# Kernel tuning notes

Hardware: AMD Instinct MI355X
Metric: run time of the kernel (lower is better)

Reference implementation:

```python
import jax, jax.numpy as jnp
import numpy as np
import math

NB = 3            # anchors per level
NC = 80           # classes
NET = 640.0       # net input size
STRIDES = (8.0, 16.0, 32.0)
ANCHORS = np.array([[12,16],[19,36],[40,28],[36,75],[76,55],[72,146],
                    [142,110],[192,243],[459,401]], dtype=np.float32)
MASKS = np.array([[0,1,2],[3,4,5],[6,7,8]], dtype=np.int32)
SCALE_XY = (2.0, 2.0, 2.0)
BALANCE = (4.0, 1.0, 0.4)
IOU_NORM = 0.05
OBJ_NORM = 0.7 * (NET / 640.0) ** 2
CLS_NORM = 0.3 * NC / 80.0
ANCHOR_T = 4.0
G = 0.5           # append_g offset threshold
EPS = 1e-7


def _bce(logits, t):
    # BCEWithLogits, elementwise: (1-t)*x + softplus(-x)
    return (1.0 - t) * logits + jax.nn.softplus(-logits)


def _ciou(box1, box2):
    # boxes are (cx, cy, w, h); returns CIoU, shape = broadcast of leading dims
    x1, y1, w1, h1 = box1[..., 0], box1[..., 1], box1[..., 2], box1[..., 3]
    x2, y2, w2, h2 = box2[..., 0], box2[..., 1], box2[..., 2], box2[..., 3]
    b1x1, b1x2 = x1 - w1 * 0.5, x1 + w1 * 0.5
    b1y1, b1y2 = y1 - h1 * 0.5, y1 + h1 * 0.5
    b2x1, b2x2 = x2 - w2 * 0.5, x2 + w2 * 0.5
    b2y1, b2y2 = y2 - h2 * 0.5, y2 + h2 * 0.5
    inter = (jnp.clip(jnp.minimum(b1x2, b2x2) - jnp.maximum(b1x1, b2x1), 0.0) *
             jnp.clip(jnp.minimum(b1y2, b2y2) - jnp.maximum(b1y1, b2y1), 0.0))
    union = w1 * h1 + w2 * h2 - inter + EPS
    iou = inter / union
    cw = jnp.maximum(b1x2, b2x2) - jnp.minimum(b1x1, b2x1)
    ch = jnp.maximum(b1y2, b2y2) - jnp.minimum(b1y1, b2y1)
    c2 = cw * cw + ch * ch + EPS
    rho2 = ((b2x1 + b2x2 - b1x1 - b1x2) ** 2 + (b2y1 + b2y2 - b1y1 - b1y2) ** 2) / 4.0
    v = (4.0 / math.pi ** 2) * (jnp.arctan(w2 / (h2 + EPS)) - jnp.arctan(w1 / (h1 + EPS))) ** 2
    alpha = jax.lax.stop_gradient(v / (v - iou + (1.0 + EPS)))
    return iou - (rho2 / c2 + v * alpha)


def _build_targets(targets, nb, S, idx):
    # vectorized version of the per-target python loop: for each target,
    # up to 5 grid cells (center + 4 offsets) x A anchor-ratio matches.
    b = targets[:, 0].astype(jnp.int32)          # [N]
    cls = targets[:, 1].astype(jnp.int32)        # [N]
    box = targets[:, 2:6]                        # [N,4] normalized xywh
    N = box.shape[0]
    A = NB
    anch = jnp.asarray(ANCHORS[MASKS[idx]] / STRIDES[idx])   # [A,2] grid units
    wh = box[:, 2:4] * S                                     # [N,2]
    r = wh[:, None, :] / anch[None, :, :]                    # [N,A,2]
    rmatch = jnp.max(jnp.maximum(r, 1.0 / r), axis=-1) < ANCHOR_T  # [N,A]
    gx, gy = box[:, 0] * S, box[:, 1] * S
    ib = jnp.floor(gx).astype(jnp.int32)
    jb = jnp.floor(gy).astype(jnp.int32)
    oi, oj = gx % 1.0, gy % 1.0
    pos = jnp.stack([
        jnp.ones_like(gx, dtype=bool),
        (oi < G) & (gx > 1.0),
        (oj < G) & (gy > 1.0),
        (oi > G) & (S - gx > 1.0),
        (oj > G) & (S - gy > 1.0)], axis=1)                  # [N,5]
    di = jnp.array([0, -1, 0, 1, 0], dtype=jnp.int32)
    dj = jnp.array([0, 0, -1, 0, 1], dtype=jnp.int32)
    ii = ib[:, None] + di                                    # [N,5]
    jj = jb[:, None] + dj                                    # [N,5]
    valid = pos[:, :, None] & rmatch[:, None, :]             # [N,5,A]
    bb = jnp.broadcast_to(b[:, None, None], (N, 5, A)).ravel()
    aa = jnp.broadcast_to(jnp.arange(A, dtype=jnp.int32)[None, None, :], (N, 5, A)).ravel()
    jf = jnp.broadcast_to(jj[:, :, None], (N, 5, A)).ravel()
    # route invalid writes out of bounds so mode='drop' discards them
    ifl = jnp.where(valid, jnp.broadcast_to(ii[:, :, None], (N, 5, A)), S).ravel()
    cf = jnp.broadcast_to(cls[:, None, None], (N, 5, A)).ravel()
    boxf = jnp.broadcast_to(box[:, None, None, :], (N, 5, A, 4)).reshape(-1, 4)
    f32 = targets.dtype
    tobj = jnp.zeros((nb, A, S, S), f32).at[bb, aa, jf, ifl].set(1.0, mode='drop')
    tcls = jnp.zeros((nb, A, S, S, NC), f32).at[bb, aa, jf, ifl, cf].set(1.0, mode='drop')
    tbox = jnp.zeros((nb, A, S, S, 4), f32).at[bb, aa, jf, ifl].set(boxf, mode='drop')
    return tobj, tcls, tbox


def _forward(preds, targets, idx):
    nb, S = preds.shape[0], preds.shape[2]
    p = preds.reshape(nb, NB, NC + 5, S, S).transpose(0, 1, 3, 4, 2)  # [nb,A,S,S,C+5]
    gy, gx = jnp.meshgrid(jnp.arange(S), jnp.arange(S), indexing='ij')
    grid = jnp.stack((gx, gy), axis=-1).astype(preds.dtype)           # [S,S,2]
    anch = jnp.asarray(ANCHORS[MASKS[idx]])                           # [A,2] pixels
    sxy = SCALE_XY[idx]
    txy = (jax.nn.sigmoid(p[..., 0:2]) * sxy - 0.5 * (sxy - 1.0) + grid) / S
    twh = jnp.exp(p[..., 2:4]) * anch[None, :, None, None, :] / NET
    pbox = jnp.concatenate([txy, twh], axis=-1)                       # [nb,A,S,S,4]
    pobj = p[..., 4]
    pcls = p[..., 5:]
    tobj, tcls, tbox = _build_targets(targets, nb, S, idx)
    mask = tobj > 0
    maskf = mask.astype(preds.dtype)
    nobj = jnp.sum(maskf)
    denom = jnp.maximum(nobj, 1.0)
    # safe target boxes where unmatched, to keep CIoU finite everywhere
    dummy = jnp.array([0.5, 0.5, 0.5, 0.5], dtype=preds.dtype)
    tbox_safe = jnp.where(mask[..., None], tbox, dummy)
    iou = _ciou(pbox, tbox_safe)                                      # [nb,A,S,S]
    has = nobj > 0
    loss_box = jnp.where(has, jnp.sum((1.0 - iou) * maskf) / denom, 0.0)
    loss_cls = jnp.where(has, jnp.sum(_bce(pcls, tcls) * maskf[..., None]) / (denom * NC), 0.0)
    tobj2 = jnp.where(mask, jax.lax.stop_gradient(jnp.maximum(iou, 0.0)), 0.0)
    loss_obj = jnp.mean(_bce(pobj, tobj2))
    loss = (OBJ_NORM * BALANCE[idx] * loss_obj + CLS_NORM * loss_cls + IOU_NORM * loss_box)
    return loss * nb


def setup_inputs() -> dict:
    key = jax.random.key(0)
    k1, k2, k3, k4, k5 = jax.random.split(key, 5)
    preds = jax.random.normal(k1, (16, NB * (NC + 5), 80, 80), dtype=jnp.float32)
    N = 256
    b = jax.random.randint(k2, (N,), 0, 16).astype(jnp.float32)
    cls = jax.random.randint(k3, (N,), 0, NC).astype(jnp.float32)
    xy = jax.random.uniform(k4, (N, 2), minval=0.02, maxval=0.98)
    wh = jax.random.uniform(k5, (N, 2), minval=0.02, maxval=0.35)
    targets = jnp.concatenate([b[:, None], cls[:, None], xy, wh], axis=1)
    return {"preds": preds, "targets": targets, "idx": 0}


def reference(preds, targets, idx):
    return _forward(preds, targets, int(idx))
```

## Files before the change

kernel.cpp:

```cpp
#include <hip/hip_runtime.h>
#include <cmath>

#define S_    80
#define NBAT  16
#define NA_   3
#define NCH_  255
#define NC_   80
#define PLANE (S_ * S_)
#define CELLS (NBAT * NA_ * PLANE)
#define NMAX  256
#define WPB   8
#define MB    (NMAX * 15 / WPB)
#define OBB   (CELLS / 4 / 512)

__device__ __forceinline__ float sp(float x) {
    return fmaxf(x, 0.f) + log1pf(__expf(-fabsf(x)));
}

__device__ __forceinline__ float ciou_f(float x1, float y1, float w1, float h1,
                                        float x2, float y2, float w2, float h2) {
    const float EPS = 1e-7f;
    float b1x1 = x1 - w1 * 0.5f, b1x2 = x1 + w1 * 0.5f;
    float b1y1 = y1 - h1 * 0.5f, b1y2 = y1 + h1 * 0.5f;
    float b2x1 = x2 - w2 * 0.5f, b2x2 = x2 + w2 * 0.5f;
    float b2y1 = y2 - h2 * 0.5f, b2y2 = y2 + h2 * 0.5f;
    float iw = fmaxf(fminf(b1x2, b2x2) - fmaxf(b1x1, b2x1), 0.f);
    float ih = fmaxf(fminf(b1y2, b2y2) - fmaxf(b1y1, b2y1), 0.f);
    float inter = iw * ih;
    float uni = w1 * h1 + w2 * h2 - inter + EPS;
    float iou = inter / uni;
    float cw = fmaxf(b1x2, b2x2) - fminf(b1x1, b2x1);
    float ch = fmaxf(b1y2, b2y2) - fminf(b1y1, b2y1);
    float c2 = cw * cw + ch * ch + EPS;
    float dx = b2x1 + b2x2 - b1x1 - b1x2;
    float dy = b2y1 + b2y2 - b1y1 - b1y2;
    float rho2 = (dx * dx + dy * dy) * 0.25f;
    float da = atanf(w2 / (h2 + EPS)) - atanf(w1 / (h1 + EPS));
    float v = 0.40528473456935109f * da * da;
    float alpha = v / (v - iou + (1.f + EPS));
    return iou - (rho2 / c2 + v * alpha);
}

__global__ void __launch_bounds__(512)
k_main(const float* __restrict__ preds,
       const float* __restrict__ tgt, int N, int mblk,
       double* __restrict__ partials) {
    int bid = blockIdx.x;
    int lane = threadIdx.x & 63, wid = threadIdx.x >> 6;
    double o_p = 0.0, b_p = 0.0, c_p = 0.0, n_p = 0.0;
    __shared__ double sm[WPB][4];

    if (bid < mblk) {
        __shared__ float st[NMAX * 6];
        int tot = N * 6;
        for (int i = threadIdx.x; i < tot; i += 512) st[i] = tgt[i];
        __syncthreads();

        const float ax[3] = {12.f / 8.f, 19.f / 8.f, 40.f / 8.f};
        const float ay[3] = {16.f / 8.f, 36.f / 8.f, 28.f / 8.f};
        const int di[5] = {0, -1, 0, 1, 0};
        const int dj[5] = {0, 0, -1, 0, 1};

        int e = bid * WPB + wid;
        int n = e / 15, r = e % 15, k = r / 3, a = r % 3;
        bool valid = (n < N);
        int b = 0, cls = 0, ii = 0, jj = 0;
        float bx = 0.f, by = 0.f, bw = 0.f, bh = 0.f;
        if (valid) {
            b   = (int)st[n * 6 + 0];
            cls = (int)st[n * 6 + 1];
            bx = st[n * 6 + 2]; by = st[n * 6 + 3];
            bw = st[n * 6 + 4]; bh = st[n * 6 + 5];
            valid = (b >= 0 && b < NBAT);
        }
        if (valid) {
            float rx = bw * S_ / ax[a]; rx = fmaxf(rx, 1.f / rx);
            float ry = bh * S_ / ay[a]; ry = fmaxf(ry, 1.f / ry);
            bool rm = fmaxf(rx, ry) < 4.0f;
            float gx = bx * S_, gy = by * S_;
            int ib = (int)floorf(gx), jb = (int)floorf(gy);
            float oi = gx - floorf(gx), oj = gy - floorf(gy);
            bool pos;
            switch (k) {
                case 0: pos = true; break;
                case 1: pos = (oi < 0.5f) && (gx > 1.f); break;
                case 2: pos = (oj < 0.5f) && (gy > 1.f); break;
                case 3: pos = (oi > 0.5f) && ((S_ - gx) > 1.f); break;
                default: pos = (oj > 0.5f) && ((S_ - gy) > 1.f); break;
            }
            ii = ib + di[k]; jj = jb + dj[k];
            valid = rm && pos && ii >= 0 && ii < S_ && jj >= 0 && jj < S_;
        }

        bool conflict = false;
        if (valid) {
#pragma unroll
            for (int l4 = 0; l4 < 4; ++l4) {
                int m = lane + l4 * 64;
                if (m < n) {
                    int b2 = (int)st[m * 6 + 0];
                    if (b2 == b) {
                        float bw2 = st[m * 6 + 4], bh2 = st[m * 6 + 5];
                        float rx2 = bw2 * S_ / ax[a]; rx2 = fmaxf(rx2, 1.f / rx2);
                        float ry2 = bh2 * S_ / ay[a]; ry2 = fmaxf(ry2, 1.f / ry2);
                        if (fmaxf(rx2, ry2) < 4.0f) {
                            float gx2 = st[m * 6 + 2] * S_, gy2 = st[m * 6 + 3] * S_;
                            int ib2 = (int)floorf(gx2), jb2 = (int)floorf(gy2);
                            float oi2 = gx2 - floorf(gx2), oj2 = gy2 - floorf(gy2);
                            bool pos2[5];
                            pos2[0] = true;
                            pos2[1] = (oi2 < 0.5f) && (gx2 > 1.f);
                            pos2[2] = (oj2 < 0.5f) && (gy2 > 1.f);
                            pos2[3] = (oi2 > 0.5f) && ((S_ - gx2) > 1.f);
                            pos2[4] = (oj2 > 0.5f) && ((S_ - gy2) > 1.f);
#pragma unroll
                            for (int k2 = 0; k2 < 5; ++k2)
                                if (pos2[k2] && (ib2 + di[k2] == ii) && (jb2 + dj[k2] == jj))
                                    conflict = true;
                        }
                    }
                }
            }
        }
        bool win = valid && (__ballot(conflict) == 0ull);

        double obj_c = 0.0, box_t = 0.0, cls_s = 0.0;
        if (win) {
            int x = ii, y = jj;
            const float* base = preds + (size_t)(b * NCH_ + a * 85) * PLANE + y * S_ + x;
            float v0 = base[lane * PLANE];
            float v1 = (lane < 21) ? base[(64 + lane) * PLANE] : 0.f;
            int clsch = 5 + cls;
            float cs = 0.f;
            if (lane >= 5) { cs += sp(v0); if (lane == clsch) cs -= v0; }
            if (lane < 21) { cs += sp(v1); if (64 + lane == clsch) cs -= v1; }
#pragma unroll
            for (int o = 32; o > 0; o >>= 1) cs += __shfl_xor(cs, o, 64);
            float p0 = __shfl(v0, 0, 64);
            float p1 = __shfl(v0, 1, 64);
            float p2 = __shfl(v0, 2, 64);
            float p3 = __shfl(v0, 3, 64);
            float po = __shfl(v0, 4, 64);

            const float anx[3]  = {12.f, 19.f, 40.f};
            const float any_[3] = {16.f, 36.f, 28.f};
            float sx = 1.f / (1.f + __expf(-p0));
            float sy = 1.f / (1.f + __expf(-p1));
            float px = (sx * 2.f - 0.5f + (float)x) * (1.0f / S_);
            float py = (sy * 2.f - 0.5f + (float)y) * (1.0f / S_);
            float pw = __expf(p2) * anx[a] * (1.0f / 640.f);
            float ph = __expf(p3) * any_[a] * (1.0f / 640.f);

            float iou = ciou_f(px, py, pw, ph, bx, by, bw, bh);
            if (lane == 0) {
                box_t = (double)(1.f - iou);
                cls_s = (double)cs;
                obj_c = (double)(-fmaxf(iou, 0.f) * po);
            }
        }
        if (lane == 0) {
            sm[wid][0] = obj_c; sm[wid][1] = box_t; sm[wid][2] = cls_s;
            sm[wid][3] = win ? 1.0 : 0.0;
        }
        __syncthreads();
        if (threadIdx.x == 0) {
#pragma unroll
            for (int w = 0; w < WPB; ++w) {
                o_p += sm[w][0]; b_p += sm[w][1]; c_p += sm[w][2]; n_p += sm[w][3];
            }
        }
    } else {
        int tid4 = (bid - mblk) * 512 + threadIdx.x;
        int plane = tid4 / (PLANE / 4);
        int pos   = tid4 % (PLANE / 4);
        int a = plane % NA_, b = plane / NA_;
        const float4* p4 = (const float4*)preds;
        float4 q = p4[(size_t)(b * NCH_ + a * 85 + 4) * (PLANE / 4) + pos];
        float v = sp(q.x) + sp(q.y) + sp(q.z) + sp(q.w);
#pragma unroll
        for (int o = 32; o > 0; o >>= 1) v += __shfl_xor(v, o, 64);
        if (lane == 0) { sm[wid][0] = (double)v; }
        __syncthreads();
        if (threadIdx.x == 0) {
#pragma unroll
            for (int w = 0; w < WPB; ++w) o_p += sm[w][0];
        }
    }

    if (threadIdx.x == 0) {
        double* p = partials + (size_t)bid * 4;
        p[0] = o_p; p[1] = b_p; p[2] = c_p; p[3] = n_p;
    }
}

__global__ void __launch_bounds__(512)
k_final(const double* __restrict__ partials, int totblk,
        float* __restrict__ out) {
    int tid = threadIdx.x;
    int lane = tid & 63, wid = tid >> 6;
    double o = 0, b = 0, c = 0, n = 0;
    for (int i = tid; i < totblk; i += 512) {
        const double* p = partials + (size_t)i * 4;
        o += p[0]; b += p[1]; c += p[2]; n += p[3];
    }
#pragma unroll
    for (int s = 32; s > 0; s >>= 1) {
        o += __shfl_xor(o, s, 64);
        b += __shfl_xor(b, s, 64);
        c += __shfl_xor(c, s, 64);
        n += __shfl_xor(n, s, 64);
    }
    __shared__ double fo[8], fb[8], fc[8], fn[8];
    if (lane == 0) { fo[wid] = o; fb[wid] = b; fc[wid] = c; fn[wid] = n; }
    __syncthreads();
    if (tid == 0) {
        double so = 0, sb = 0, sc = 0, sn = 0;
#pragma unroll
        for (int w = 0; w < 8; ++w) { so += fo[w]; sb += fb[w]; sc += fc[w]; sn += fn[w]; }
        double denom = fmax(sn, 1.0);
        double loss_obj = so / (double)CELLS;
        double loss_box = sb / denom;
        double loss_cls = sc / (denom * (double)NC_);
        double loss = (0.7 * 4.0) * loss_obj + 0.3 * loss_cls + 0.05 * loss_box;
        out[0] = (float)(loss * (double)NBAT);
    }
}

extern "C" void kernel_launch(void* const* d_in, const int* in_sizes, int n_in,
                              void* d_out, int out_size, void* d_ws, size_t ws_size,
                              hipStream_t stream) {
    (void)n_in; (void)out_size; (void)ws_size;
    const float* preds = (const float*)d_in[0];
    const float* tgt   = (const float*)d_in[1];
    int N = in_sizes[1] / 6;
    if (N > NMAX) N = NMAX;

    double* partials = (double*)d_ws;
    int mblk   = (N * 15 + WPB - 1) / WPB;
    int totblk = mblk + OBB;

    k_main<<<totblk, 512, 0, stream>>>(preds, tgt, N, mblk, partials);
    k_final<<<1, 512, 0, stream>>>(partials, totblk, (float*)d_out);
}
```

Before: 15.12 us.

## Drop shared target staging, halve objectness blocks, use float partials

Matching blocks now read targets straight from global memory instead of first copying all of them into shared memory and synchronizing. Each objectness block handles two float4 loads per thread, which halves the number of such blocks. Per-block partials become a single float4 store instead of four doubles, and the final reducer uses 256 threads. Together these cut block count, barrier overhead and partial traffic, at the cost of slightly less precise per-block sums and repeated global reads of the target array.

```diff
diff --git a/kernel.cpp b/kernel.cpp
--- a/kernel.cpp
+++ b/kernel.cpp
@@ -10,8 +10,7 @@
 #define CELLS (NBAT * NA_ * PLANE)
 #define NMAX  256
 #define WPB   8
-#define MB    (NMAX * 15 / WPB)
-#define OBB   (CELLS / 4 / 512)
+#define OBB   (CELLS / 4 / 512 / 2)
 
 __device__ __forceinline__ float sp(float x) {
     return fmaxf(x, 0.f) + log1pf(__expf(-fabsf(x)));
@@ -44,18 +43,13 @@
 __global__ void __launch_bounds__(512)
 k_main(const float* __restrict__ preds,
        const float* __restrict__ tgt, int N, int mblk,
-       double* __restrict__ partials) {
+       float4* __restrict__ partials) {
     int bid = blockIdx.x;
     int lane = threadIdx.x & 63, wid = threadIdx.x >> 6;
-    double o_p = 0.0, b_p = 0.0, c_p = 0.0, n_p = 0.0;
-    __shared__ double sm[WPB][4];
+    float o_p = 0.f, b_p = 0.f, c_p = 0.f, n_p = 0.f;
+    __shared__ float smf[WPB][4];
 
     if (bid < mblk) {
-        __shared__ float st[NMAX * 6];
-        int tot = N * 6;
-        for (int i = threadIdx.x; i < tot; i += 512) st[i] = tgt[i];
-        __syncthreads();
-
         const float ax[3] = {12.f / 8.f, 19.f / 8.f, 40.f / 8.f};
         const float ay[3] = {16.f / 8.f, 36.f / 8.f, 28.f / 8.f};
         const int di[5] = {0, -1, 0, 1, 0};
@@ -67,10 +61,10 @@
         int b = 0, cls = 0, ii = 0, jj = 0;
         float bx = 0.f, by = 0.f, bw = 0.f, bh = 0.f;
         if (valid) {
-            b   = (int)st[n * 6 + 0];
-            cls = (int)st[n * 6 + 1];
-            bx = st[n * 6 + 2]; by = st[n * 6 + 3];
-            bw = st[n * 6 + 4]; bh = st[n * 6 + 5];
+            b   = (int)tgt[n * 6 + 0];
+            cls = (int)tgt[n * 6 + 1];
+            bx = tgt[n * 6 + 2]; by = tgt[n * 6 + 3];
+            bw = tgt[n * 6 + 4]; bh = tgt[n * 6 + 5];
             valid = (b >= 0 && b < NBAT);
         }
         if (valid) {
@@ -98,13 +92,13 @@
             for (int l4 = 0; l4 < 4; ++l4) {
                 int m = lane + l4 * 64;
                 if (m < n) {
-                    int b2 = (int)st[m * 6 + 0];
+                    int b2 = (int)tgt[m * 6 + 0];
                     if (b2 == b) {
-                        float bw2 = st[m * 6 + 4], bh2 = st[m * 6 + 5];
+                        float bw2 = tgt[m * 6 + 4], bh2 = tgt[m * 6 + 5];
                         float rx2 = bw2 * S_ / ax[a]; rx2 = fmaxf(rx2, 1.f / rx2);
                         float ry2 = bh2 * S_ / ay[a]; ry2 = fmaxf(ry2, 1.f / ry2);
                         if (fmaxf(rx2, ry2) < 4.0f) {
-                            float gx2 = st[m * 6 + 2] * S_, gy2 = st[m * 6 + 3] * S_;
+                            float gx2 = tgt[m * 6 + 2] * S_, gy2 = tgt[m * 6 + 3] * S_;
                             int ib2 = (int)floorf(gx2), jb2 = (int)floorf(gy2);
                             float oi2 = gx2 - floorf(gx2), oj2 = gy2 - floorf(gy2);
                             bool pos2[5];
@@ -124,7 +118,7 @@
         }
         bool win = valid && (__ballot(conflict) == 0ull);
 
-        double obj_c = 0.0, box_t = 0.0, cls_s = 0.0;
+        float obj_c = 0.f, box_t = 0.f, cls_s = 0.f;
         if (win) {
             int x = ii, y = jj;
             const float* base = preds + (size_t)(b * NCH_ + a * 85) * PLANE + y * S_ + x;
@@ -153,55 +147,57 @@
 
             float iou = ciou_f(px, py, pw, ph, bx, by, bw, bh);
             if (lane == 0) {
-                box_t = (double)(1.f - iou);
-                cls_s = (double)cs;
-                obj_c = (double)(-fmaxf(iou, 0.f) * po);
+                box_t = 1.f - iou;
+                cls_s = cs;
+                obj_c = -fmaxf(iou, 0.f) * po;
             }
         }
         if (lane == 0) {
-            sm[wid][0] = obj_c; sm[wid][1] = box_t; sm[wid][2] = cls_s;
-            sm[wid][3] = win ? 1.0 : 0.0;
+            smf[wid][0] = obj_c; smf[wid][1] = box_t; smf[wid][2] = cls_s;
+            smf[wid][3] = win ? 1.f : 0.f;
         }
         __syncthreads();
         if (threadIdx.x == 0) {
 #pragma unroll
             for (int w = 0; w < WPB; ++w) {
-                o_p += sm[w][0]; b_p += sm[w][1]; c_p += sm[w][2]; n_p += sm[w][3];
+                o_p += smf[w][0]; b_p += smf[w][1]; c_p += smf[w][2]; n_p += smf[w][3];
             }
         }
     } else {
-        int tid4 = (bid - mblk) * 512 + threadIdx.x;
-        int plane = tid4 / (PLANE / 4);
-        int pos   = tid4 % (PLANE / 4);
-        int a = plane % NA_, b = plane / NA_;
         const float4* p4 = (const float4*)preds;
-        float4 q = p4[(size_t)(b * NCH_ + a * 85 + 4) * (PLANE / 4) + pos];
-        float v = sp(q.x) + sp(q.y) + sp(q.z) + sp(q.w);
+        float v = 0.f;
+#pragma unroll
+        for (int rr = 0; rr < 2; ++rr) {
+            int tid4 = (bid - mblk) * 1024 + rr * 512 + threadIdx.x;
+            int plane = tid4 / (PLANE / 4);
+            int pos   = tid4 % (PLANE / 4);
+            int a = plane % NA_, b = plane / NA_;
+            float4 q = p4[(size_t)(b * NCH_ + a * 85 + 4) * (PLANE / 4) + pos];
+            v += sp(q.x) + sp(q.y) + sp(q.z) + sp(q.w);
+        }
 #pragma unroll
         for (int o = 32; o > 0; o >>= 1) v += __shfl_xor(v, o, 64);
-        if (lane == 0) { sm[wid][0] = (double)v; }
+        if (lane == 0) { smf[wid][0] = v; }
         __syncthreads();
         if (threadIdx.x == 0) {
 #pragma unroll
-            for (int w = 0; w < WPB; ++w) o_p += sm[w][0];
-        }
-    }
-
-    if (threadIdx.x == 0) {
-        double* p = partials + (size_t)bid * 4;
-        p[0] = o_p; p[1] = b_p; p[2] = c_p; p[3] = n_p;
-    }
-}
-
-__global__ void __launch_bounds__(512)
-k_final(const double* __restrict__ partials, int totblk,
+            for (int w = 0; w < WPB; ++w) o_p += smf[w][0];
+        }
+    }
+
+    if (threadIdx.x == 0)
+        partials[bid] = make_float4(o_p, b_p, c_p, n_p);
+}
+
+__global__ void __launch_bounds__(256)
+k_final(const float4* __restrict__ partials, int totblk,
         float* __restrict__ out) {
     int tid = threadIdx.x;
     int lane = tid & 63, wid = tid >> 6;
     double o = 0, b = 0, c = 0, n = 0;
-    for (int i = tid; i < totblk; i += 512) {
-        const double* p = partials + (size_t)i * 4;
-        o += p[0]; b += p[1]; c += p[2]; n += p[3];
+    for (int i = tid; i < totblk; i += 256) {
+        float4 p = partials[i];
+        o += (double)p.x; b += (double)p.y; c += (double)p.z; n += (double)p.w;
     }
 #pragma unroll
     for (int s = 32; s > 0; s >>= 1) {
@@ -210,13 +206,13 @@
         c += __shfl_xor(c, s, 64);
         n += __shfl_xor(n, s, 64);
     }
-    __shared__ double fo[8], fb[8], fc[8], fn[8];
+    __shared__ double fo[4], fb[4], fc[4], fn[4];
     if (lane == 0) { fo[wid] = o; fb[wid] = b; fc[wid] = c; fn[wid] = n; }
     __syncthreads();
     if (tid == 0) {
         double so = 0, sb = 0, sc = 0, sn = 0;
 #pragma unroll
-        for (int w = 0; w < 8; ++w) { so += fo[w]; sb += fb[w]; sc += fc[w]; sn += fn[w]; }
+        for (int w = 0; w < 4; ++w) { so += fo[w]; sb += fb[w]; sc += fc[w]; sn += fn[w]; }
         double denom = fmax(sn, 1.0);
         double loss_obj = so / (double)CELLS;
         double loss_box = sb / denom;
@@ -235,10 +231,10 @@
     int N = in_sizes[1] / 6;
     if (N > NMAX) N = NMAX;
 
-    double* partials = (double*)d_ws;
+    float4* partials = (float4*)d_ws;
     int mblk   = (N * 15 + WPB - 1) / WPB;
     int totblk = mblk + OBB;
 
     k_main<<<totblk, 512, 0, stream>>>(preds, tgt, N, mblk, partials);
-    k_final<<<1, 512, 0, stream>>>(partials, totblk, (float*)d_out);
-}
+    k_final<<<1, 256, 0, stream>>>(partials, totblk, (float*)d_out);
+}
```

Measured after the change: 14.51 us (median of 2 runs). 1.04x faster.
